# Kernel tuning notes

Hardware: AMD Instinct MI355X
Metric: run time of the kernel (lower is better)

The kernel has to match this reference:

```python
import jax, jax.numpy as jnp
import numpy as np

B, S, D = 8, 4096, 1024
EPS = 1e-8  # torch F.cosine_similarity default eps


def setup_inputs() -> dict:
    key = jax.random.key(0)
    kx, kwq, kbq, kwk, kbk = jax.random.split(key, 5)
    bound = 1.0 / np.sqrt(D)  # torch nn.Linear default init
    return {
        "x": jax.random.normal(kx, (B, S, D), dtype=jnp.float32),
        "Wq": jax.random.uniform(kwq, (D, D), jnp.float32, -bound, bound),
        "bq": jax.random.uniform(kbq, (D,), jnp.float32, -bound, bound),
        "Wk": jax.random.uniform(kwk, (D, D), jnp.float32, -bound, bound),
        "bk": jax.random.uniform(kbk, (D,), jnp.float32, -bound, bound),
    }


def reference(x, Wq, bq, Wk, bk):
    # ---- RoutingModule ----
    q = jnp.einsum("bsd,ed->bse", x, Wq) + bq                      # [B,S,D]
    x_roll = jnp.roll(x, shift=1, axis=1)                           # roll along seq
    k = jnp.einsum("bsd,ed->bse", x_roll, Wk) + bk                  # [B,S,D]
    qn = q / jnp.maximum(jnp.linalg.norm(q, axis=-1, keepdims=True), EPS)
    kn = k / jnp.maximum(jnp.linalg.norm(k, axis=-1, keepdims=True), EPS)
    cosine_sim = jnp.sum(qn * kn, axis=-1)                          # [B,S]
    p = 0.5 * (1.0 - cosine_sim)
    p = p.at[:, 0].set(1.0)
    b = (p >= 0.5).astype(x.dtype)                                  # [B,S]

    # ---- ragged compaction into padded buffer ----
    # Stable argsort moves selected positions to the front, preserving order.
    order = jnp.argsort(1.0 - b, axis=1)                            # [B,S] int
    gathered = jnp.take_along_axis(x, order[:, :, None], axis=1)    # [B,S,D]
    counts = jnp.sum(b, axis=1).astype(jnp.int32)                   # [B]
    valid = jnp.arange(S)[None, :] < counts[:, None]                # [B,S]
    # Padded to S (static max possible length) for jit-compatibility; torch
    # trims to the batch max, but all rows beyond each count are zeros here too.
    selected_padded = jnp.where(valid[:, :, None], gathered, 0.0)   # [B,S,D]
    return selected_padded, p, b
```

## Files before the change

### kernel.cpp

```cpp
#include <hip/hip_runtime.h>
#include <stdint.h>

#define Bb 8
#define Ss 4096
#define Dd 1024
#define Mm (Bb*Ss)
#define Kk 1024

typedef _Float16 half8 __attribute__((ext_vector_type(8)));
typedef _Float16 half4v __attribute__((ext_vector_type(4)));
typedef float f32x4 __attribute__((ext_vector_type(4)));

#define LO_SCALE 2048.0f
#define INV_LO_SCALE (1.0f/2048.0f)

__device__ __forceinline__ void gld_lds16(const void* g, void* l) {
  __builtin_amdgcn_global_load_lds(
      (const __attribute__((address_space(1))) unsigned int*)g,
      (__attribute__((address_space(3))) unsigned int*)l, 16, 0, 0);
}

__global__ void split_w3(const float* __restrict__ Gp, const float* __restrict__ Wq,
                         const float* __restrict__ Wk,
                         _Float16* __restrict__ Gh, _Float16* __restrict__ Gl,
                         _Float16* __restrict__ Wh) {
  const int which = blockIdx.y;
  const int i = blockIdx.x * 256 + threadIdx.x;
  float4 v;
  if (which == 0) {
    float4 v0 = ((const float4*)Gp)[i];
    float4 v1 = ((const float4*)(Gp + (size_t)Dd * Dd))[i];
    float4 v2 = ((const float4*)(Gp + (size_t)2 * Dd * Dd))[i];
    float4 v3 = ((const float4*)(Gp + (size_t)3 * Dd * Dd))[i];
    v.x = (v0.x + v1.x) + (v2.x + v3.x);
    v.y = (v0.y + v1.y) + (v2.y + v3.y);
    v.z = (v0.z + v1.z) + (v2.z + v3.z);
    v.w = (v0.w + v1.w) + (v2.w + v3.w);
  } else {
    const float* src = (which == 1) ? Wq : Wk;
    v = ((const float4*)src)[i];
  }
  _Float16 h0 = (_Float16)v.x, h1 = (_Float16)v.y, h2 = (_Float16)v.z, h3 = (_Float16)v.w;
  if (which == 0) {
    _Float16 l0 = (_Float16)((v.x - (float)h0) * LO_SCALE);
    _Float16 l1 = (_Float16)((v.y - (float)h1) * LO_SCALE);
    _Float16 l2 = (_Float16)((v.z - (float)h2) * LO_SCALE);
    _Float16 l3 = (_Float16)((v.w - (float)h3) * LO_SCALE);
    ((half4v*)Gh)[i] = (half4v){h0, h1, h2, h3};
    ((half4v*)Gl)[i] = (half4v){l0, l1, l2, l3};
  } else {
    _Float16* hi = (which == 1) ? Wh : Wh + (size_t)Dd * Dd;
    ((half4v*)hi)[i] = (half4v){h0, h1, h2, h3};
  }
}

__global__ void split_x(const float* __restrict__ X, const float* __restrict__ u,
                        const float* __restrict__ v,
                        _Float16* __restrict__ Xh, _Float16* __restrict__ Xl,
                        float* __restrict__ a_u, float* __restrict__ a_v) {
  const int s = blockIdx.x * 4 + (threadIdx.x >> 6);
  const int lane = threadIdx.x & 63;
  float au = 0.f, av = 0.f;
#pragma unroll
  for (int c = 0; c < 4; ++c) {
    const int e = c * 256 + lane * 4;
    float4 xv = *(const float4*)&X[(size_t)s * Dd + e];
    float4 uv = *(const float4*)&u[e];
    float4 vv = *(const float4*)&v[e];
    _Float16 h0 = (_Float16)xv.x, h1 = (_Float16)xv.y, h2 = (_Float16)xv.z, h3 = (_Float16)xv.w;
    _Float16 l0 = (_Float16)((xv.x - (float)h0) * LO_SCALE);
    _Float16 l1 = (_Float16)((xv.y - (float)h1) * LO_SCALE);
    _Float16 l2 = (_Float16)((xv.z - (float)h2) * LO_SCALE);
    _Float16 l3 = (_Float16)((xv.w - (float)h3) * LO_SCALE);
    *(half4v*)&Xh[(size_t)s * Dd + e] = (half4v){h0, h1, h2, h3};
    *(half4v*)&Xl[(size_t)s * Dd + e] = (half4v){l0, l1, l2, l3};
    au += uv.x * xv.x + uv.y * xv.y + uv.z * xv.z + uv.w * xv.w;
    av += vv.x * xv.x + vv.y * xv.y + vv.z * xv.z + vv.w * xv.w;
  }
#pragma unroll
  for (int off = 32; off > 0; off >>= 1) {
    au += __shfl_xor(au, off);
    av += __shfl_xor(av, off);
  }
  if (lane == 0) { a_u[s] = au; a_v[s] = av; }
}

__global__ __launch_bounds__(256)
void gemm_g_part(const float* __restrict__ Wq, const float* __restrict__ Wk,
                 float* __restrict__ Gp) {
  __shared__ float As[16][64];
  __shared__ float Bs[16][64];
  const int t = threadIdx.x;
  const int m0 = blockIdx.y * 64, n0 = blockIdx.x * 64;
  const int kbase = blockIdx.z * 256;
  float acc[4][4];
#pragma unroll
  for (int a = 0; a < 4; ++a)
#pragma unroll
    for (int b = 0; b < 4; ++b) acc[a][b] = 0.f;
  for (int kc = 0; kc < 16; ++kc) {
    const int k0 = kbase + kc * 16;
#pragma unroll
    for (int l = 0; l < 4; ++l) {
      const int idx = l * 256 + t;
      const int kk = idx >> 6, mm = idx & 63;
      As[kk][mm] = Wq[(size_t)(k0 + kk) * Dd + m0 + mm];
      Bs[kk][mm] = Wk[(size_t)(k0 + kk) * Dd + n0 + mm];
    }
    __syncthreads();
    const int tm = (t & 15) * 4, tn = (t >> 4) * 4;
#pragma unroll
    for (int k = 0; k < 16; ++k) {
      float4 a4 = *(const float4*)&As[k][tm];
      float4 b4 = *(const float4*)&Bs[k][tn];
      const float aa[4] = {a4.x, a4.y, a4.z, a4.w};
      const float bb[4] = {b4.x, b4.y, b4.z, b4.w};
#pragma unroll
      for (int a = 0; a < 4; ++a)
#pragma unroll
        for (int b = 0; b < 4; ++b) acc[a][b] += aa[a] * bb[b];
    }
    __syncthreads();
  }
  float* dst = Gp + (size_t)blockIdx.z * Dd * Dd;
  const int tm = (t & 15) * 4, tn = (t >> 4) * 4;
#pragma unroll
  for (int a = 0; a < 4; ++a)
#pragma unroll
    for (int b = 0; b < 4; ++b)
      dst[(size_t)(m0 + tm + a) * Dd + n0 + tn + b] = acc[a][b];
}

__global__ void uvc_part(const float* __restrict__ Wq, const float* __restrict__ Wk,
                         const float* __restrict__ bq, const float* __restrict__ bk,
                         float* __restrict__ up, float* __restrict__ vp,
                         float* __restrict__ c) {
  const int bx = blockIdx.x;
  if (bx == 32) {
    const int lane = threadIdx.x;
    if (lane >= 64) return;
    float a = 0.f;
#pragma unroll
    for (int i = 0; i < 16; ++i) a += bq[lane * 16 + i] * bk[lane * 16 + i];
#pragma unroll
    for (int off = 32; off > 0; off >>= 1) a += __shfl_xor(a, off);
    if (lane == 0) *c = a;
    return;
  }
  const int echunk = bx & 3;
  const int which = (bx >> 2) & 1;
  const int dchunk = bx >> 3;
  const int d = dchunk * 256 + threadIdx.x;
  const float* W = which ? Wq : Wk;
  const float* bb = which ? bk : bq;
  float acc = 0.f;
  const int e0 = echunk * 256;
#pragma unroll 4
  for (int e = e0; e < e0 + 256; ++e) acc += bb[e] * W[(size_t)e * Dd + d];
  float* dst = which ? vp : up;
  dst[(size_t)echunk * Dd + d] = acc;
}

__global__ void uvc_reduce(const float* __restrict__ up, const float* __restrict__ vp,
                           float* __restrict__ u, float* __restrict__ v) {
  const int d = threadIdx.x;
  u[d] = (up[d] + up[Dd + d]) + (up[2 * Dd + d] + up[3 * Dd + d]);
  v[d] = (vp[d] + vp[Dd + d]) + (vp[2 * Dd + d] + vp[3 * Dd + d]);
}

__global__ __launch_bounds__(256, 2)
void gemm_fused(const _Float16* __restrict__ Ah, const _Float16* __restrict__ Al,
                const _Float16* __restrict__ Gh, const _Float16* __restrict__ Gl,
                const _Float16* __restrict__ Wh,
                const float* __restrict__ X,
                const float* __restrict__ bq, const float* __restrict__ bk,
                float* __restrict__ pd, float* __restrict__ pn) {
  __shared__ __align__(16) _Float16 smem[4 * 128 * 32];
  const int tid = threadIdx.x;
  const int wave = tid >> 6, lane = tid & 63;
  const int m0 = blockIdx.y * 128;
  const int wm = (wave >> 1) * 64, wn = (wave & 1) * 64;
  const int fr = lane & 15, g = lane >> 4;

  if (blockIdx.x < 8) {
    _Float16* AsH = smem;
    _Float16* AsL = smem + 4096;
    _Float16* BsH = smem + 8192;
    _Float16* BsL = smem + 12288;
    const int n0 = blockIdx.x * 128;
    const int srow = lane >> 2, c8 = lane & 3;
    f32x4 accH[4][4], accX[4][4];
#pragma unroll
    for (int i = 0; i < 4; ++i)
#pragma unroll
      for (int j = 0; j < 4; ++j) {
        accH[i][j] = (f32x4){0.f, 0.f, 0.f, 0.f};
        accX[i][j] = (f32x4){0.f, 0.f, 0.f, 0.f};
      }
    for (int kt = 0; kt < Kk / 32; ++kt) {
      const int k0 = kt * 32;
#pragma unroll
      for (int it = 0; it < 2; ++it) {
        const int R = wave * 32 + it * 16 + srow;
        const int sg = c8 ^ ((R >> 2) & 3);
        const int ldsoff = (wave * 32 + it * 16) * 32;
        const size_t ga = (size_t)(m0 + R) * Kk + k0 + sg * 8;
        const size_t gb = (size_t)(n0 + R) * Kk + k0 + sg * 8;
        gld_lds16(Ah + ga, &AsH[ldsoff]);
        gld_lds16(Al + ga, &AsL[ldsoff]);
        gld_lds16(Gh + gb, &BsH[ldsoff]);
        gld_lds16(Gl + gb, &BsL[ldsoff]);
      }
      __syncthreads();
      half8 bh[4], bl[4];
#pragma unroll
      for (int j = 0; j < 4; ++j) {
        const int R = wn + 16 * j + fr;
        const int slot = g ^ ((R >> 2) & 3);
        bh[j] = *(const half8*)&BsH[R * 32 + slot * 8];
        bl[j] = *(const half8*)&BsL[R * 32 + slot * 8];
      }
#pragma unroll
      for (int i = 0; i < 4; ++i) {
        const int R = wm + 16 * i + fr;
        const int slot = g ^ ((R >> 2) & 3);
        half8 ah = *(const half8*)&AsH[R * 32 + slot * 8];
        half8 al = *(const half8*)&AsL[R * 32 + slot * 8];
#pragma unroll
        for (int j = 0; j < 4; ++j) {
          accH[i][j] = __builtin_amdgcn_mfma_f32_16x16x32_f16(ah, bh[j], accH[i][j], 0, 0, 0);
          accX[i][j] = __builtin_amdgcn_mfma_f32_16x16x32_f16(ah, bl[j], accX[i][j], 0, 0, 0);
          accX[i][j] = __builtin_amdgcn_mfma_f32_16x16x32_f16(al, bh[j], accX[i][j], 0, 0, 0);
        }
      }
      __syncthreads();
    }
    const int quad = lane >> 4;
    const int slot = blockIdx.x * 2 + (wave & 1);
#pragma unroll
    for (int i = 0; i < 4; ++i) {
#pragma unroll
      for (int r = 0; r < 4; ++r) {
        const int s = m0 + wm + 16 * i + quad * 4 + r;
        const int t = s + 1;
        float dsum = 0.f;
        if ((t & (Ss - 1)) != 0) {
          const float* xrow = X + (size_t)t * Dd + n0 + wn;
#pragma unroll
          for (int j = 0; j < 4; ++j) {
            float yv = accH[i][j][r] + accX[i][j][r] * INV_LO_SCALE;
            dsum += yv * xrow[16 * j + fr];
          }
        }
        dsum += __shfl_xor(dsum, 1);
        dsum += __shfl_xor(dsum, 2);
        dsum += __shfl_xor(dsum, 4);
        dsum += __shfl_xor(dsum, 8);
        if (fr == 0 && ((t & (Ss - 1)) != 0))
          pd[(size_t)slot * Mm + t] = dsum;
      }
    }
  } else {
    _Float16* NA = smem;
    _Float16* NB = smem + 8192;
    const int n0 = (blockIdx.x - 8) * 128;
    f32x4 acc[4][4];
#pragma unroll
    for (int i = 0; i < 4; ++i)
#pragma unroll
      for (int j = 0; j < 4; ++j) acc[i][j] = (f32x4){0.f, 0.f, 0.f, 0.f};
    const int srow8 = lane >> 3, s8 = lane & 7;
    for (int kt = 0; kt < Kk / 64; ++kt) {
      const int k0 = kt * 64;
#pragma unroll
      for (int it = 0; it < 4; ++it) {
        const int R = wave * 32 + it * 8 + srow8;
        const int gcol = k0 + ((s8 ^ (R & 7)) * 8);
        const int ldsoff = (wave * 32 + it * 8) * 64;
        gld_lds16(Ah + (size_t)(m0 + R) * Kk + gcol, &NA[ldsoff]);
        gld_lds16(Wh + (size_t)(n0 + R) * Kk + gcol, &NB[ldsoff]);
      }
      __syncthreads();
#pragma unroll
      for (int kk = 0; kk < 2; ++kk) {
        const int gg = kk * 4 + g;
        half8 bh[4];
#pragma unroll
        for (int j = 0; j < 4; ++j) {
          const int R = wn + 16 * j + fr;
          bh[j] = *(const half8*)&NB[R * 64 + (gg ^ (R & 7)) * 8];
        }
#pragma unroll
        for (int i = 0; i < 4; ++i) {
          const int R = wm + 16 * i + fr;
          half8 ah = *(const half8*)&NA[R * 64 + (gg ^ (R & 7)) * 8];
#pragma unroll
          for (int j = 0; j < 4; ++j)
            acc[i][j] = __builtin_amdgcn_mfma_f32_16x16x32_f16(ah, bh[j], acc[i][j], 0, 0, 0);
        }
      }
      __syncthreads();
    }
    const int quad = lane >> 4;
    float bias_j[4];
#pragma unroll
    for (int j = 0; j < 4; ++j) {
      const int n = n0 + wn + 16 * j + fr;
      bias_j[j] = (n < Dd) ? bq[n] : bk[n - Dd];
    }
    const int slot = (blockIdx.x - 8) * 2 + (wave & 1);
#pragma unroll
    for (int i = 0; i < 4; ++i) {
#pragma unroll
      for (int r = 0; r < 4; ++r) {
        float vsum = 0.f;
#pragma unroll
        for (int j = 0; j < 4; ++j) {
          float q = acc[i][j][r] + bias_j[j];
          vsum += q * q;
        }
        vsum += __shfl_xor(vsum, 1);
        vsum += __shfl_xor(vsum, 2);
        vsum += __shfl_xor(vsum, 4);
        vsum += __shfl_xor(vsum, 8);
        if (fr == 0)
          pn[(size_t)slot * Mm + (m0 + wm + 16 * i + quad * 4 + r)] = vsum;
      }
    }
  }
}

__global__ void cos_final(const float* __restrict__ pd, const float* __restrict__ pn,
                          const float* __restrict__ a_u, const float* __restrict__ a_v,
                          const float* __restrict__ cptr,
                          float* __restrict__ p_out, float* __restrict__ b_out) {
  const int s = blockIdx.x * 256 + threadIdx.x;
  if ((s & (Ss - 1)) == 0) { p_out[s] = 1.0f; b_out[s] = 1.0f; return; }
  float dot = a_u[s - 1] + a_v[s] + *cptr;
#pragma unroll
  for (int sl = 0; sl < 16; ++sl) dot += pd[(size_t)sl * Mm + s];
  float nq = 0.f, nk = 0.f;
#pragma unroll
  for (int sl = 0; sl < 16; ++sl) nq += pn[(size_t)sl * Mm + s];
#pragma unroll
  for (int sl = 16; sl < 32; ++sl) nk += pn[(size_t)sl * Mm + (s - 1)];
  float denom = fmaxf(sqrtf(nq), 1e-8f) * fmaxf(sqrtf(nk), 1e-8f);
  float cs = dot / denom;
  float p = 0.5f * (1.0f - cs);
  p_out[s] = p;
  b_out[s] = (p >= 0.5f) ? 1.0f : 0.0f;
}

__global__ void scan_flags(const float* __restrict__ b_out,
                           int* __restrict__ sel, int* __restrict__ counts) {
  const int b = blockIdx.x;
  const int tid = threadIdx.x;
  const int lane = tid & 63;
  const int w = tid >> 6;
  __shared__ int wtot[4];
  int running = 0;
  for (int c = 0; c < Ss / 256; ++c) {
    const int i = c * 256 + tid;
    const bool f = b_out[b * Ss + i] != 0.0f;
    unsigned long long m = __ballot(f);
    int pre = __popcll(m & ((1ull << lane) - 1ull));
    if (lane == 0) wtot[w] = __popcll(m);
    __syncthreads();
    int woff = 0;
#pragma unroll
    for (int ww = 0; ww < 4; ++ww)
      if (ww < w) woff += wtot[ww];
    int tot = wtot[0] + wtot[1] + wtot[2] + wtot[3];
    if (f) sel[b * Ss + running + woff + pre] = i;
    running += tot;
    __syncthreads();
  }
  if (tid == 0) counts[b] = running;
}

__global__ void write_out(const float* __restrict__ x, const int* __restrict__ sel,
                          const int* __restrict__ counts, float* __restrict__ out) {
  const int blk = blockIdx.x;
  const int b = blk >> 12;
  const int r = blk & (Ss - 1);
  const int tid = threadIdx.x;
  float4 v = {0.f, 0.f, 0.f, 0.f};
  if (r < counts[b]) {
    const int src = sel[b * Ss + r];
    v = *(const float4*)&x[((size_t)b * Ss + src) * Dd + tid * 4];
  }
  *(float4*)&out[(size_t)blk * Dd + tid * 4] = v;
}

extern "C" void kernel_launch(void* const* d_in, const int* in_sizes, int n_in,
                              void* d_out, int out_size, void* d_ws, size_t ws_size,
                              hipStream_t stream) {
  const float* x  = (const float*)d_in[0];
  const float* Wq = (const float*)d_in[1];
  const float* bq = (const float*)d_in[2];
  const float* Wk = (const float*)d_in[3];
  const float* bk = (const float*)d_in[4];
  float* out = (float*)d_out;

  uint8_t* w = (uint8_t*)d_ws;
  _Float16* Xh = (_Float16*)w;   w += (size_t)Mm * Kk * 2;
  _Float16* Xl = (_Float16*)w;   w += (size_t)Mm * Kk * 2;
  float*    Gp = (float*)w;      w += (size_t)4 * Dd * Dd * 4;
  _Float16* Gh = (_Float16*)w;   w += (size_t)Dd * Dd * 2;
  _Float16* Gl = (_Float16*)w;   w += (size_t)Dd * Dd * 2;
  _Float16* Wh = (_Float16*)w;   w += (size_t)2 * Dd * Dd * 2;
  float* pd = (float*)w;         w += (size_t)16 * Mm * 4;
  float* pn = (float*)w;         w += (size_t)32 * Mm * 4;
  float* a_u = (float*)w;        w += (size_t)Mm * 4;
  float* a_v = (float*)w;        w += (size_t)Mm * 4;
  float* up  = (float*)w;        w += (size_t)4 * Dd * 4;
  float* vp  = (float*)w;        w += (size_t)4 * Dd * 4;
  float* u   = (float*)w;        w += Dd * 4;
  float* v   = (float*)w;        w += Dd * 4;
  float* cpt = (float*)w;        w += 64;
  int*   sel = (int*)w;          w += (size_t)Mm * 4;
  int*   counts = (int*)w;       w += 64;

  float* p_out = out + (size_t)Mm * Dd;
  float* b_out = p_out + Mm;

  gemm_g_part<<<dim3(16, 16, 4), 256, 0, stream>>>(Wq, Wk, Gp);
  uvc_part<<<33, 256, 0, stream>>>(Wq, Wk, bq, bk, up, vp, cpt);
  uvc_reduce<<<1, 1024, 0, stream>>>(up, vp, u, v);
  split_x<<<Mm / 4, 256, 0, stream>>>(x, u, v, Xh, Xl, a_u, a_v);
  split_w3<<<dim3((Dd * Dd / 4) / 256, 3), 256, 0, stream>>>(Gp, Wq, Wk, Gh, Gl, Wh);
  gemm_fused<<<dim3(24, Mm / 128), 256, 0, stream>>>(Xh, Xl, Gh, Gl, Wh, x, bq, bk, pd, pn);
  cos_final<<<Mm / 256, 256, 0, stream>>>(pd, pn, a_u, a_v, cpt, p_out, b_out);
  scan_flags<<<Bb, 256, 0, stream>>>(b_out, sel, counts);
  write_out<<<Mm, 256, 0, stream>>>(x, sel, counts, out);
}
```

Baseline: 781.9 us.

## Split fused GEMM into separate dot and norm kernels with K=64 tiles

Splits the heterogeneous fused GEMM (dot-product blocks and norm blocks sharing one launch and one register/LDS budget) into two kernels. The dot GEMM now uses 64-wide K tiles with an 8-way XOR swizzle, halving the barrier count per K. The norm GEMM gets its own launch bounds, allowing three blocks per CU. It also folds the uvc_reduce kernel into split_x and widens scan_flags to 1024 threads with the loads issued up front. The trade-offs are an extra kernel launch and twice the LDS for the dot kernel, which may lower its occupancy.

```diff
diff --git a/kernel.cpp b/kernel.cpp
--- a/kernel.cpp
+++ b/kernel.cpp
@@ -54,8 +54,8 @@
   }
 }
 
-__global__ void split_x(const float* __restrict__ X, const float* __restrict__ u,
-                        const float* __restrict__ v,
+__global__ void split_x(const float* __restrict__ X, const float* __restrict__ up,
+                        const float* __restrict__ vp,
                         _Float16* __restrict__ Xh, _Float16* __restrict__ Xl,
                         float* __restrict__ a_u, float* __restrict__ a_v) {
   const int s = blockIdx.x * 4 + (threadIdx.x >> 6);
@@ -65,8 +65,14 @@
   for (int c = 0; c < 4; ++c) {
     const int e = c * 256 + lane * 4;
     float4 xv = *(const float4*)&X[(size_t)s * Dd + e];
-    float4 uv = *(const float4*)&u[e];
-    float4 vv = *(const float4*)&v[e];
+    float4 uv = {0.f, 0.f, 0.f, 0.f}, vv = {0.f, 0.f, 0.f, 0.f};
+#pragma unroll
+    for (int z = 0; z < 4; ++z) {
+      float4 a = *(const float4*)&up[(size_t)z * Dd + e];
+      float4 b = *(const float4*)&vp[(size_t)z * Dd + e];
+      uv.x += a.x; uv.y += a.y; uv.z += a.z; uv.w += a.w;
+      vv.x += b.x; vv.y += b.y; vv.z += b.z; vv.w += b.w;
+    }
     _Float16 h0 = (_Float16)xv.x, h1 = (_Float16)xv.y, h2 = (_Float16)xv.z, h3 = (_Float16)xv.w;
     _Float16 l0 = (_Float16)((xv.x - (float)h0) * LO_SCALE);
     _Float16 l1 = (_Float16)((xv.y - (float)h1) * LO_SCALE);
@@ -161,71 +167,63 @@
   dst[(size_t)echunk * Dd + d] = acc;
 }
 
-__global__ void uvc_reduce(const float* __restrict__ up, const float* __restrict__ vp,
-                           float* __restrict__ u, float* __restrict__ v) {
-  const int d = threadIdx.x;
-  u[d] = (up[d] + up[Dd + d]) + (up[2 * Dd + d] + up[3 * Dd + d]);
-  v[d] = (vp[d] + vp[Dd + d]) + (vp[2 * Dd + d] + vp[3 * Dd + d]);
-}
-
 __global__ __launch_bounds__(256, 2)
-void gemm_fused(const _Float16* __restrict__ Ah, const _Float16* __restrict__ Al,
-                const _Float16* __restrict__ Gh, const _Float16* __restrict__ Gl,
-                const _Float16* __restrict__ Wh,
-                const float* __restrict__ X,
-                const float* __restrict__ bq, const float* __restrict__ bk,
-                float* __restrict__ pd, float* __restrict__ pn) {
-  __shared__ __align__(16) _Float16 smem[4 * 128 * 32];
+void gemm_dot(const _Float16* __restrict__ Ah, const _Float16* __restrict__ Al,
+              const _Float16* __restrict__ Gh, const _Float16* __restrict__ Gl,
+              const float* __restrict__ X, float* __restrict__ pd) {
+  __shared__ __align__(16) _Float16 smem[4 * 128 * 64];
+  _Float16* AsH = smem;
+  _Float16* AsL = smem + 8192;
+  _Float16* BsH = smem + 16384;
+  _Float16* BsL = smem + 24576;
   const int tid = threadIdx.x;
   const int wave = tid >> 6, lane = tid & 63;
-  const int m0 = blockIdx.y * 128;
+  const int m0 = blockIdx.y * 128, n0 = blockIdx.x * 128;
   const int wm = (wave >> 1) * 64, wn = (wave & 1) * 64;
   const int fr = lane & 15, g = lane >> 4;
-
-  if (blockIdx.x < 8) {
-    _Float16* AsH = smem;
-    _Float16* AsL = smem + 4096;
-    _Float16* BsH = smem + 8192;
-    _Float16* BsL = smem + 12288;
-    const int n0 = blockIdx.x * 128;
-    const int srow = lane >> 2, c8 = lane & 3;
-    f32x4 accH[4][4], accX[4][4];
-#pragma unroll
-    for (int i = 0; i < 4; ++i)
-#pragma unroll
-      for (int j = 0; j < 4; ++j) {
-        accH[i][j] = (f32x4){0.f, 0.f, 0.f, 0.f};
-        accX[i][j] = (f32x4){0.f, 0.f, 0.f, 0.f};
-      }
-    for (int kt = 0; kt < Kk / 32; ++kt) {
-      const int k0 = kt * 32;
-#pragma unroll
-      for (int it = 0; it < 2; ++it) {
-        const int R = wave * 32 + it * 16 + srow;
-        const int sg = c8 ^ ((R >> 2) & 3);
-        const int ldsoff = (wave * 32 + it * 16) * 32;
-        const size_t ga = (size_t)(m0 + R) * Kk + k0 + sg * 8;
-        const size_t gb = (size_t)(n0 + R) * Kk + k0 + sg * 8;
-        gld_lds16(Ah + ga, &AsH[ldsoff]);
-        gld_lds16(Al + ga, &AsL[ldsoff]);
-        gld_lds16(Gh + gb, &BsH[ldsoff]);
-        gld_lds16(Gl + gb, &BsL[ldsoff]);
-      }
-      __syncthreads();
+  const int srow8 = lane >> 3, s8 = lane & 7;
+
+  f32x4 accH[4][4], accX[4][4];
+#pragma unroll
+  for (int i = 0; i < 4; ++i)
+#pragma unroll
+    for (int j = 0; j < 4; ++j) {
+      accH[i][j] = (f32x4){0.f, 0.f, 0.f, 0.f};
+      accX[i][j] = (f32x4){0.f, 0.f, 0.f, 0.f};
+    }
+
+  for (int kt = 0; kt < Kk / 64; ++kt) {
+    const int k0 = kt * 64;
+#pragma unroll
+    for (int it = 0; it < 4; ++it) {
+      const int R = wave * 32 + it * 8 + srow8;
+      const int gcol = k0 + ((s8 ^ (R & 7)) * 8);
+      const int ldsoff = (wave * 32 + it * 8) * 64;
+      const size_t ga = (size_t)(m0 + R) * Kk + gcol;
+      const size_t gb = (size_t)(n0 + R) * Kk + gcol;
+      gld_lds16(Ah + ga, &AsH[ldsoff]);
+      gld_lds16(Al + ga, &AsL[ldsoff]);
+      gld_lds16(Gh + gb, &BsH[ldsoff]);
+      gld_lds16(Gl + gb, &BsL[ldsoff]);
+    }
+    __syncthreads();
+#pragma unroll
+    for (int kk = 0; kk < 2; ++kk) {
+      const int gg = kk * 4 + g;
       half8 bh[4], bl[4];
 #pragma unroll
       for (int j = 0; j < 4; ++j) {
         const int R = wn + 16 * j + fr;
-        const int slot = g ^ ((R >> 2) & 3);
-        bh[j] = *(const half8*)&BsH[R * 32 + slot * 8];
-        bl[j] = *(const half8*)&BsL[R * 32 + slot * 8];
+        const int sl = (gg ^ (R & 7)) * 8;
+        bh[j] = *(const half8*)&BsH[R * 64 + sl];
+        bl[j] = *(const half8*)&BsL[R * 64 + sl];
       }
 #pragma unroll
       for (int i = 0; i < 4; ++i) {
         const int R = wm + 16 * i + fr;
-        const int slot = g ^ ((R >> 2) & 3);
-        half8 ah = *(const half8*)&AsH[R * 32 + slot * 8];
-        half8 al = *(const half8*)&AsL[R * 32 + slot * 8];
+        const int sl = (gg ^ (R & 7)) * 8;
+        half8 ah = *(const half8*)&AsH[R * 64 + sl];
+        half8 al = *(const half8*)&AsL[R * 64 + sl];
 #pragma unroll
         for (int j = 0; j < 4; ++j) {
           accH[i][j] = __builtin_amdgcn_mfma_f32_16x16x32_f16(ah, bh[j], accH[i][j], 0, 0, 0);
@@ -233,99 +231,111 @@
           accX[i][j] = __builtin_amdgcn_mfma_f32_16x16x32_f16(al, bh[j], accX[i][j], 0, 0, 0);
         }
       }
-      __syncthreads();
-    }
-    const int quad = lane >> 4;
-    const int slot = blockIdx.x * 2 + (wave & 1);
-#pragma unroll
-    for (int i = 0; i < 4; ++i) {
-#pragma unroll
-      for (int r = 0; r < 4; ++r) {
-        const int s = m0 + wm + 16 * i + quad * 4 + r;
-        const int t = s + 1;
-        float dsum = 0.f;
-        if ((t & (Ss - 1)) != 0) {
-          const float* xrow = X + (size_t)t * Dd + n0 + wn;
-#pragma unroll
-          for (int j = 0; j < 4; ++j) {
-            float yv = accH[i][j][r] + accX[i][j][r] * INV_LO_SCALE;
-            dsum += yv * xrow[16 * j + fr];
-          }
+    }
+    __syncthreads();
+  }
+  const int quad = lane >> 4;
+  const int slot = blockIdx.x * 2 + (wave & 1);
+#pragma unroll
+  for (int i = 0; i < 4; ++i) {
+#pragma unroll
+    for (int r = 0; r < 4; ++r) {
+      const int s = m0 + wm + 16 * i + quad * 4 + r;
+      const int t = s + 1;
+      float dsum = 0.f;
+      if ((t & (Ss - 1)) != 0) {
+        const float* xrow = X + (size_t)t * Dd + n0 + wn;
+#pragma unroll
+        for (int j = 0; j < 4; ++j) {
+          float yv = accH[i][j][r] + accX[i][j][r] * INV_LO_SCALE;
+          dsum += yv * xrow[16 * j + fr];
         }
-        dsum += __shfl_xor(dsum, 1);
-        dsum += __shfl_xor(dsum, 2);
-        dsum += __shfl_xor(dsum, 4);
-        dsum += __shfl_xor(dsum, 8);
-        if (fr == 0 && ((t & (Ss - 1)) != 0))
-          pd[(size_t)slot * Mm + t] = dsum;
-      }
-    }
-  } else {
-    _Float16* NA = smem;
-    _Float16* NB = smem + 8192;
-    const int n0 = (blockIdx.x - 8) * 128;
-    f32x4 acc[4][4];
-#pragma unroll
-    for (int i = 0; i < 4; ++i)
-#pragma unroll
-      for (int j = 0; j < 4; ++j) acc[i][j] = (f32x4){0.f, 0.f, 0.f, 0.f};
-    const int srow8 = lane >> 3, s8 = lane & 7;
-    for (int kt = 0; kt < Kk / 64; ++kt) {
-      const int k0 = kt * 64;
-#pragma unroll
-      for (int it = 0; it < 4; ++it) {
-        const int R = wave * 32 + it * 8 + srow8;
-        const int gcol = k0 + ((s8 ^ (R & 7)) * 8);
-        const int ldsoff = (wave * 32 + it * 8) * 64;
-        gld_lds16(Ah + (size_t)(m0 + R) * Kk + gcol, &NA[ldsoff]);
-        gld_lds16(Wh + (size_t)(n0 + R) * Kk + gcol, &NB[ldsoff]);
-      }
-      __syncthreads();
-#pragma unroll
-      for (int kk = 0; kk < 2; ++kk) {
-        const int gg = kk * 4 + g;
-        half8 bh[4];
-#pragma unroll
-        for (int j = 0; j < 4; ++j) {
-          const int R = wn + 16 * j + fr;
-          bh[j] = *(const half8*)&NB[R * 64 + (gg ^ (R & 7)) * 8];
-        }
-#pragma unroll
-        for (int i = 0; i < 4; ++i) {
-          const int R = wm + 16 * i + fr;
-          half8 ah = *(const half8*)&NA[R * 64 + (gg ^ (R & 7)) * 8];
-#pragma unroll
-          for (int j = 0; j < 4; ++j)
-            acc[i][j] = __builtin_amdgcn_mfma_f32_16x16x32_f16(ah, bh[j], acc[i][j], 0, 0, 0);
-        }
-      }
-      __syncthreads();
-    }
-    const int quad = lane >> 4;
-    float bias_j[4];
-#pragma unroll
-    for (int j = 0; j < 4; ++j) {
-      const int n = n0 + wn + 16 * j + fr;
-      bias_j[j] = (n < Dd) ? bq[n] : bk[n - Dd];
-    }
-    const int slot = (blockIdx.x - 8) * 2 + (wave & 1);
-#pragma unroll
-    for (int i = 0; i < 4; ++i) {
-#pragma unroll
-      for (int r = 0; r < 4; ++r) {
-        float vsum = 0.f;
-#pragma unroll
-        for (int j = 0; j < 4; ++j) {
-          float q = acc[i][j][r] + bias_j[j];
-          vsum += q * q;
-        }
-        vsum += __shfl_xor(vsum, 1);
-        vsum += __shfl_xor(vsum, 2);
-        vsum += __shfl_xor(vsum, 4);
-        vsum += __shfl_xor(vsum, 8);
-        if (fr == 0)
-          pn[(size_t)slot * Mm + (m0 + wm + 16 * i + quad * 4 + r)] = vsum;
-      }
+      }
+      dsum += __shfl_xor(dsum, 1);
+      dsum += __shfl_xor(dsum, 2);
+      dsum += __shfl_xor(dsum, 4);
+      dsum += __shfl_xor(dsum, 8);
+      if (fr == 0 && ((t & (Ss - 1)) != 0))
+        pd[(size_t)slot * Mm + t] = dsum;
+    }
+  }
+}
+
+__global__ __launch_bounds__(256, 3)
+void gemm_norm(const _Float16* __restrict__ Ah, const _Float16* __restrict__ Wh,
+               const float* __restrict__ bq, const float* __restrict__ bk,
+               float* __restrict__ pn) {
+  __shared__ __align__(16) _Float16 smem[2 * 128 * 64];
+  _Float16* NA = smem;
+  _Float16* NB = smem + 8192;
+  const int tid = threadIdx.x;
+  const int wave = tid >> 6, lane = tid & 63;
+  const int m0 = blockIdx.y * 128, n0 = blockIdx.x * 128;
+  const int wm = (wave >> 1) * 64, wn = (wave & 1) * 64;
+  const int fr = lane & 15, g = lane >> 4;
+  const int srow8 = lane >> 3, s8 = lane & 7;
+
+  f32x4 acc[4][4];
+#pragma unroll
+  for (int i = 0; i < 4; ++i)
+#pragma unroll
+    for (int j = 0; j < 4; ++j) acc[i][j] = (f32x4){0.f, 0.f, 0.f, 0.f};
+
+  for (int kt = 0; kt < Kk / 64; ++kt) {
+    const int k0 = kt * 64;
+#pragma unroll
+    for (int it = 0; it < 4; ++it) {
+      const int R = wave * 32 + it * 8 + srow8;
+      const int gcol = k0 + ((s8 ^ (R & 7)) * 8);
+      const int ldsoff = (wave * 32 + it * 8) * 64;
+      gld_lds16(Ah + (size_t)(m0 + R) * Kk + gcol, &NA[ldsoff]);
+      gld_lds16(Wh + (size_t)(n0 + R) * Kk + gcol, &NB[ldsoff]);
+    }
+    __syncthreads();
+#pragma unroll
+    for (int kk = 0; kk < 2; ++kk) {
+      const int gg = kk * 4 + g;
+      half8 bh[4];
+#pragma unroll
+      for (int j = 0; j < 4; ++j) {
+        const int R = wn + 16 * j + fr;
+        bh[j] = *(const half8*)&NB[R * 64 + (gg ^ (R & 7)) * 8];
+      }
+#pragma unroll
+      for (int i = 0; i < 4; ++i) {
+        const int R = wm + 16 * i + fr;
+        half8 ah = *(const half8*)&NA[R * 64 + (gg ^ (R & 7)) * 8];
+#pragma unroll
+        for (int j = 0; j < 4; ++j)
+          acc[i][j] = __builtin_amdgcn_mfma_f32_16x16x32_f16(ah, bh[j], acc[i][j], 0, 0, 0);
+      }
+    }
+    __syncthreads();
+  }
+  const int quad = lane >> 4;
+  float bias_j[4];
+#pragma unroll
+  for (int j = 0; j < 4; ++j) {
+    const int n = n0 + wn + 16 * j + fr;
+    bias_j[j] = (n < Dd) ? bq[n] : bk[n - Dd];
+  }
+  const int slot = blockIdx.x * 2 + (wave & 1);
+#pragma unroll
+  for (int i = 0; i < 4; ++i) {
+#pragma unroll
+    for (int r = 0; r < 4; ++r) {
+      float vsum = 0.f;
+#pragma unroll
+      for (int j = 0; j < 4; ++j) {
+        float q = acc[i][j][r] + bias_j[j];
+        vsum += q * q;
+      }
+      vsum += __shfl_xor(vsum, 1);
+      vsum += __shfl_xor(vsum, 2);
+      vsum += __shfl_xor(vsum, 4);
+      vsum += __shfl_xor(vsum, 8);
+      if (fr == 0)
+        pn[(size_t)slot * Mm + (m0 + wm + 16 * i + quad * 4 + r)] = vsum;
     }
   }
 }
@@ -351,27 +361,33 @@
   b_out[s] = (p >= 0.5f) ? 1.0f : 0.0f;
 }
 
-__global__ void scan_flags(const float* __restrict__ b_out,
-                           int* __restrict__ sel, int* __restrict__ counts) {
+__global__ __launch_bounds__(1024)
+void scan_flags(const float* __restrict__ b_out,
+                int* __restrict__ sel, int* __restrict__ counts) {
   const int b = blockIdx.x;
   const int tid = threadIdx.x;
   const int lane = tid & 63;
   const int w = tid >> 6;
-  __shared__ int wtot[4];
+  __shared__ int wtot[16];
+  float fv[4];
+#pragma unroll
+  for (int c = 0; c < 4; ++c) fv[c] = b_out[b * Ss + c * 1024 + tid];
   int running = 0;
-  for (int c = 0; c < Ss / 256; ++c) {
-    const int i = c * 256 + tid;
-    const bool f = b_out[b * Ss + i] != 0.0f;
+#pragma unroll
+  for (int c = 0; c < 4; ++c) {
+    const bool f = fv[c] != 0.0f;
     unsigned long long m = __ballot(f);
     int pre = __popcll(m & ((1ull << lane) - 1ull));
     if (lane == 0) wtot[w] = __popcll(m);
     __syncthreads();
-    int woff = 0;
-#pragma unroll
-    for (int ww = 0; ww < 4; ++ww)
-      if (ww < w) woff += wtot[ww];
-    int tot = wtot[0] + wtot[1] + wtot[2] + wtot[3];
-    if (f) sel[b * Ss + running + woff + pre] = i;
+    int woff = 0, tot = 0;
+#pragma unroll
+    for (int ww = 0; ww < 16; ++ww) {
+      int t = wtot[ww];
+      if (ww < w) woff += t;
+      tot += t;
+    }
+    if (f) sel[b * Ss + running + woff + pre] = c * 1024 + tid;
     running += tot;
     __syncthreads();
   }
@@ -415,8 +431,6 @@
   float* a_v = (float*)w;        w += (size_t)Mm * 4;
   float* up  = (float*)w;        w += (size_t)4 * Dd * 4;
   float* vp  = (float*)w;        w += (size_t)4 * Dd * 4;
-  float* u   = (float*)w;        w += Dd * 4;
-  float* v   = (float*)w;        w += Dd * 4;
   float* cpt = (float*)w;        w += 64;
   int*   sel = (int*)w;          w += (size_t)Mm * 4;
   int*   counts = (int*)w;       w += 64;
@@ -426,11 +440,11 @@
 
   gemm_g_part<<<dim3(16, 16, 4), 256, 0, stream>>>(Wq, Wk, Gp);
   uvc_part<<<33, 256, 0, stream>>>(Wq, Wk, bq, bk, up, vp, cpt);
-  uvc_reduce<<<1, 1024, 0, stream>>>(up, vp, u, v);
-  split_x<<<Mm / 4, 256, 0, stream>>>(x, u, v, Xh, Xl, a_u, a_v);
+  split_x<<<Mm / 4, 256, 0, stream>>>(x, up, vp, Xh, Xl, a_u, a_v);
   split_w3<<<dim3((Dd * Dd / 4) / 256, 3), 256, 0, stream>>>(Gp, Wq, Wk, Gh, Gl, Wh);
-  gemm_fused<<<dim3(24, Mm / 128), 256, 0, stream>>>(Xh, Xl, Gh, Gl, Wh, x, bq, bk, pd, pn);
+  gemm_norm<<<dim3(2 * Dd / 128, Mm / 128), 256, 0, stream>>>(Xh, Wh, bq, bk, pn);
+  gemm_dot<<<dim3(Dd / 128, Mm / 128), 256, 0, stream>>>(Xh, Xl, Gh, Gl, x, pd);
   cos_final<<<Mm / 256, 256, 0, stream>>>(pd, pn, a_u, a_v, cpt, p_out, b_out);
-  scan_flags<<<Bb, 256, 0, stream>>>(b_out, sel, counts);
+  scan_flags<<<Bb, 1024, 0, stream>>>(b_out, sel, counts);
   write_out<<<Mm, 256, 0, stream>>>(x, sel, counts, out);
 }
```

Result: faster. 718.7 us (-8.1%).
